# Performance work log

Hardware: AMD Instinct MI355X
Metric: run time of the kernel (lower is better)

## Reference

```python
import jax, jax.numpy as jnp
import numpy as np

N = 50000
BN_EPS = 1e-5


def gcn_conv(x, W, b, src, dst, n):
    # PyG GCNConv: linear transform, add self-loops, symmetric normalization,
    # aggregate messages from src (edge_index[0]) at dst (edge_index[1]).
    x = x @ W
    loop = jnp.arange(n, dtype=src.dtype)
    s = jnp.concatenate([src, loop])
    d = jnp.concatenate([dst, loop])
    ones = jnp.ones(s.shape[0], dtype=x.dtype)
    deg = jax.ops.segment_sum(ones, d, num_segments=n)
    dinv = jnp.where(deg > 0, jax.lax.rsqrt(deg), 0.0)
    norm = dinv[s] * dinv[d]                      # [E+N]
    msg = x[s] * norm[:, None]                    # gather + scale
    out = jax.ops.segment_sum(msg, d, num_segments=n)  # scatter-add
    return out + b


def batch_norm(x, gamma, beta):
    mean = jnp.mean(x, axis=0)
    var = jnp.mean(jnp.square(x - mean), axis=0)  # biased, as torch BN
    return (x - mean) * jax.lax.rsqrt(var + BN_EPS) * gamma + beta


def setup_inputs() -> dict:
    key = jax.random.key(0)
    ks = jax.random.split(key, 4)
    DIN, DH, DOUT, E = 128, 128, 40, 800000
    node_feat = jax.random.normal(ks[0], (N, DIN), dtype=jnp.float32)
    edge_index = jax.random.randint(ks[1], (2, E), 0, N, dtype=jnp.int32)
    W1 = jax.random.normal(ks[2], (DIN, DH), dtype=jnp.float32) / np.sqrt(DIN)
    W2 = jax.random.normal(ks[3], (DH, DOUT), dtype=jnp.float32) / np.sqrt(DH)
    return {
        "node_feat": node_feat,
        "W1": W1,
        "b1": jnp.zeros((DH,), jnp.float32),
        "gamma1": jnp.ones((DH,), jnp.float32),
        "beta1": jnp.zeros((DH,), jnp.float32),
        "W2": W2,
        "b2": jnp.zeros((DOUT,), jnp.float32),
        "edge_index": edge_index,
    }


def reference(node_feat, W1, b1, gamma1, beta1, W2, b2, edge_index):
    src, dst = edge_index[0], edge_index[1]
    x = gcn_conv(node_feat, W1, b1, src, dst, N)
    x = batch_norm(x, gamma1, beta1)
    x = jax.nn.relu(x)
    # dropout is identity at inference
    x = gcn_conv(x, W2, b2, src, dst, N)
    return x
```

## Files before the change

### kernel.cpp

```cpp
#include <hip/hip_runtime.h>

#define NN 50000
#define DIN 128
#define DH  128
#define DOUT 40
#define BN_EPS 1e-5f

__device__ __forceinline__ void atomAddF(float* p, float v) {
  unsafeAtomicAdd(p, v);
}

__global__ void k_deg(const int* __restrict__ dst, int* __restrict__ deg, int E) {
  int e = blockIdx.x * blockDim.x + threadIdx.x;
  if (e < E) atomicAdd(&deg[dst[e]], 1);
}

__global__ void k_off(const int* __restrict__ deg, int* __restrict__ off,
                      int* __restrict__ cur, float* __restrict__ dinv,
                      int* __restrict__ counter) {
  int i = blockIdx.x * 256 + threadIdx.x;
  int lane = threadIdx.x & 63;
  int d = (i < NN) ? deg[i] : 0;
  int pre = d;
#pragma unroll
  for (int o = 1; o < 64; o <<= 1) {
    int v = __shfl_up(pre, o);
    if (lane >= o) pre += v;
  }
  int tot = __shfl(pre, 63);
  int base = 0;
  if (lane == 63) base = atomicAdd(counter, tot);
  base = __shfl(base, 63);
  int o0 = base + pre - d;
  if (i < NN) {
    off[i] = o0; cur[i] = o0;
    dinv[i] = rsqrtf((float)d + 1.0f);
  }
}

__global__ void k_fill(const int* __restrict__ src, const int* __restrict__ dst,
                       int* __restrict__ cur, int* __restrict__ csr, int E) {
  int e = blockIdx.x * blockDim.x + threadIdx.x;
  if (e >= E) return;
  int pos = atomicAdd(&cur[dst[e]], 1);
  csr[pos] = src[e];
}

__global__ __launch_bounds__(256) void k_gemm1(const float* __restrict__ X,
                                               const float* __restrict__ W,
                                               const float* __restrict__ dinv,
                                               float* __restrict__ Y) {
  int t = threadIdx.x;
  int tx = t & 31;
  int ty = t >> 5;
  int r0 = blockIdx.x * 64 + ty * 8;
  int c0 = tx * 4;
  const float4* W4 = (const float4*)W;

  const float* xp[8];
#pragma unroll
  for (int r = 0; r < 8; ++r) {
    int row = r0 + r;
    if (row >= NN) row = NN - 1;
    xp[r] = X + (size_t)row * DIN;
  }

  float acc[8][4] = {};
  for (int k = 0; k < DIN; k += 4) {
    float4 w0 = W4[(k + 0) * 32 + tx];
    float4 w1 = W4[(k + 1) * 32 + tx];
    float4 w2 = W4[(k + 2) * 32 + tx];
    float4 w3 = W4[(k + 3) * 32 + tx];
#pragma unroll
    for (int r = 0; r < 8; ++r) {
      float4 xv = *(const float4*)(xp[r] + k);
      acc[r][0] = fmaf(xv.x, w0.x, fmaf(xv.y, w1.x, fmaf(xv.z, w2.x, fmaf(xv.w, w3.x, acc[r][0]))));
      acc[r][1] = fmaf(xv.x, w0.y, fmaf(xv.y, w1.y, fmaf(xv.z, w2.y, fmaf(xv.w, w3.y, acc[r][1]))));
      acc[r][2] = fmaf(xv.x, w0.z, fmaf(xv.y, w1.z, fmaf(xv.z, w2.z, fmaf(xv.w, w3.z, acc[r][2]))));
      acc[r][3] = fmaf(xv.x, w0.w, fmaf(xv.y, w1.w, fmaf(xv.z, w2.w, fmaf(xv.w, w3.w, acc[r][3]))));
    }
  }
#pragma unroll
  for (int r = 0; r < 8; ++r) {
    int row = r0 + r;
    if (row < NN) {
      float dv = dinv[row];
      *(float4*)(Y + (size_t)row * DH + c0) =
          make_float4(acc[r][0] * dv, acc[r][1] * dv, acc[r][2] * dv, acc[r][3] * dv);
    }
  }
}

__global__ __launch_bounds__(256) void k_pull1(
    const int* __restrict__ off, const int* __restrict__ deg,
    const int* __restrict__ csr, const float* __restrict__ Y1,
    const float* __restrict__ dinv, const float* __restrict__ b1,
    float* __restrict__ Z, float* __restrict__ colsum,
    float* __restrict__ colsumsq) {
  __shared__ float s_sum[4][128], s_sq[4][128];
  int t = threadIdx.x, lane = t & 63, wid = t >> 6;
  const float2* Y = (const float2*)Y1;
  float bx = b1[2 * lane], by = b1[2 * lane + 1];
  float sx = 0.f, sy = 0.f, qx = 0.f, qy = 0.f;
  int n0 = blockIdx.x * 16 + wid * 4;
  for (int u = 0; u < 4; ++u) {
    int n = n0 + u;
    float2 acc = Y[(size_t)n * 64 + lane];
    int o = off[n], dg = deg[n];
    for (int base = 0; base < dg; base += 64) {
      int cnt = min(64, dg - base);
      int myidx = (base + lane < dg) ? csr[o + base + lane] : 0;
      for (int k = 0; k < cnt; ++k) {
        int sN = __shfl(myidx, k);
        float2 y = Y[(size_t)sN * 64 + lane];
        acc.x += y.x; acc.y += y.y;
      }
    }
    float dn = dinv[n];
    float zx = fmaf(dn, acc.x, bx);
    float zy = fmaf(dn, acc.y, by);
    ((float2*)Z)[(size_t)n * 64 + lane] = make_float2(zx, zy);
    sx += zx; sy += zy; qx += zx * zx; qy += zy * zy;
  }
  s_sum[wid][2 * lane] = sx; s_sum[wid][2 * lane + 1] = sy;
  s_sq[wid][2 * lane]  = qx; s_sq[wid][2 * lane + 1]  = qy;
  __syncthreads();
  if (t < 128) {
    atomAddF(&colsum[t],   s_sum[0][t] + s_sum[1][t] + s_sum[2][t] + s_sum[3][t]);
    atomAddF(&colsumsq[t], s_sq[0][t] + s_sq[1][t] + s_sq[2][t] + s_sq[3][t]);
  }
}

__global__ void k_bn(const float* __restrict__ colsum, const float* __restrict__ colsumsq,
                     const float* __restrict__ gamma, const float* __restrict__ beta,
                     float* __restrict__ scale, float* __restrict__ shift) {
  int j = threadIdx.x;
  float mean = colsum[j] * (1.0f / NN);
  float var  = colsumsq[j] * (1.0f / NN) - mean * mean;
  float sc = gamma[j] * rsqrtf(var + BN_EPS);
  scale[j] = sc;
  shift[j] = beta[j] - mean * sc;
}

__global__ __launch_bounds__(256) void k_gemm2(const float* __restrict__ Z,
                                               const float* __restrict__ W2,
                                               const float* __restrict__ scale,
                                               const float* __restrict__ shift,
                                               const float* __restrict__ dinv,
                                               float* __restrict__ Y2) {
  int t = threadIdx.x;
  if (t >= 250) return;
  int tx = t % 10;
  int ty = t / 10;
  int r0 = blockIdx.x * 100 + ty * 4;
  int c0 = tx * 4;
  const float4* W4  = (const float4*)W2;
  const float4* sc4 = (const float4*)scale;
  const float4* sh4 = (const float4*)shift;

  const float* zp[4];
#pragma unroll
  for (int r = 0; r < 4; ++r) zp[r] = Z + (size_t)(r0 + r) * DH;

  float acc[4][4] = {};
  for (int k4 = 0; k4 < DH / 4; ++k4) {
    int k = k4 * 4;
    float4 sc = sc4[k4], sh = sh4[k4];
    float4 w0 = W4[(k + 0) * 10 + tx];
    float4 w1 = W4[(k + 1) * 10 + tx];
    float4 w2 = W4[(k + 2) * 10 + tx];
    float4 w3 = W4[(k + 3) * 10 + tx];
#pragma unroll
    for (int r = 0; r < 4; ++r) {
      float4 zv = *(const float4*)(zp[r] + k);
      float x0 = fmaxf(fmaf(zv.x, sc.x, sh.x), 0.f);
      float x1 = fmaxf(fmaf(zv.y, sc.y, sh.y), 0.f);
      float x2 = fmaxf(fmaf(zv.z, sc.z, sh.z), 0.f);
      float x3 = fmaxf(fmaf(zv.w, sc.w, sh.w), 0.f);
      acc[r][0] = fmaf(x0, w0.x, fmaf(x1, w1.x, fmaf(x2, w2.x, fmaf(x3, w3.x, acc[r][0]))));
      acc[r][1] = fmaf(x0, w0.y, fmaf(x1, w1.y, fmaf(x2, w2.y, fmaf(x3, w3.y, acc[r][1]))));
      acc[r][2] = fmaf(x0, w0.z, fmaf(x1, w1.z, fmaf(x2, w2.z, fmaf(x3, w3.z, acc[r][2]))));
      acc[r][3] = fmaf(x0, w0.w, fmaf(x1, w1.w, fmaf(x2, w2.w, fmaf(x3, w3.w, acc[r][3]))));
    }
  }
#pragma unroll
  for (int r = 0; r < 4; ++r) {
    int row = r0 + r;
    float dv = dinv[row];
    *(float4*)(Y2 + (size_t)row * DOUT + c0) =
        make_float4(acc[r][0] * dv, acc[r][1] * dv, acc[r][2] * dv, acc[r][3] * dv);
  }
}

__global__ __launch_bounds__(256) void k_pull2(
    const int* __restrict__ off, const int* __restrict__ deg,
    const int* __restrict__ csr, const float* __restrict__ Y2,
    const float* __restrict__ dinv, const float* __restrict__ b2,
    float* __restrict__ out) {
  int t = threadIdx.x, lane = t & 63, wid = t >> 6;
  bool act = lane < DOUT;
  float bv = act ? b2[lane] : 0.f;
  int n0 = blockIdx.x * 16 + wid * 4;
  for (int u = 0; u < 4; ++u) {
    int n = n0 + u;
    float acc = act ? Y2[(size_t)n * DOUT + lane] : 0.f;
    int o = off[n], dg = deg[n];
    for (int base = 0; base < dg; base += 64) {
      int cnt = min(64, dg - base);
      int myidx = (base + lane < dg) ? csr[o + base + lane] : 0;
      for (int k = 0; k < cnt; ++k) {
        int sN = __shfl(myidx, k);
        if (act) acc += Y2[(size_t)sN * DOUT + lane];
      }
    }
    if (act) out[(size_t)n * DOUT + lane] = fmaf(dinv[n], acc, bv);
  }
}

extern "C" void kernel_launch(void* const* d_in, const int* in_sizes, int n_in,
                              void* d_out, int out_size, void* d_ws, size_t ws_size,
                              hipStream_t stream) {
  const float* X     = (const float*)d_in[0];
  const float* W1    = (const float*)d_in[1];
  const float* b1    = (const float*)d_in[2];
  const float* gamma = (const float*)d_in[3];
  const float* beta  = (const float*)d_in[4];
  const float* W2    = (const float*)d_in[5];
  const float* b2    = (const float*)d_in[6];
  const int*   edges = (const int*)d_in[7];
  int E = in_sizes[7] / 2;
  const int* src = edges;
  const int* dst = edges + E;

  int E4 = (E + 3) & ~3;
  int* i_deg = (int*)d_ws;
  int* i_off = i_deg + 50048;
  int* i_cur = i_off + 50048;
  int* i_cnt = i_cur + 50016;
  int* i_csr = i_cur + 50048;
  float* f_dinv = (float*)(i_csr + E4);
  float* f_Y1   = f_dinv + 50048;
  float* f_Z    = f_Y1 + (size_t)NN * DH;
  float* f_st   = f_Z + (size_t)NN * DH;
  float* f_Y2   = f_Y1;

  hipMemsetAsync(i_deg, 0, 50000 * sizeof(int), stream);
  hipMemsetAsync(i_cnt, 0, sizeof(int), stream);
  hipMemsetAsync(f_st, 0, 256 * sizeof(float), stream);

  k_deg <<<(E + 255) / 256, 256, 0, stream>>>(dst, i_deg, E);
  k_off <<<(NN + 255) / 256, 256, 0, stream>>>(i_deg, i_off, i_cur, f_dinv, i_cnt);
  k_fill<<<(E + 255) / 256, 256, 0, stream>>>(src, dst, i_cur, i_csr, E);
  k_gemm1<<<(NN + 63) / 64, 256, 0, stream>>>(X, W1, f_dinv, f_Y1);
  k_pull1<<<NN / 16, 256, 0, stream>>>(i_off, i_deg, i_csr, f_Y1, f_dinv, b1,
                                       f_Z, f_st, f_st + 128);
  k_bn<<<1, 128, 0, stream>>>(f_st, f_st + 128, gamma, beta, f_st + 256, f_st + 384);
  k_gemm2<<<500, 256, 0, stream>>>(f_Z, W2, f_st + 256, f_st + 384, f_dinv, f_Y2);
  k_pull2<<<NN / 16, 256, 0, stream>>>(i_off, i_deg, i_csr, f_Y2, f_dinv, b2,
                                       (float*)d_out);
}
```

Before: 432.5 us.

## Store GEMM outputs as bf16 and unroll edge gathers with scalar CSR loads

Both GEMMs now write their dinv-scaled feature rows as bf16 instead of fp32. This halves the bytes the pull kernels gather for every edge. The pull loops drop the shuffle-broadcast of neighbor indices in favor of wave-uniform CSR reads via readfirstlane, unrolled by 8 so several gathers are in flight at once. The cost is bf16 rounding of intermediate messages, which could loosen accuracy against the fp32 reference.

```diff
diff --git a/kernel.cpp b/kernel.cpp
--- a/kernel.cpp
+++ b/kernel.cpp
@@ -8,6 +8,20 @@
 
 __device__ __forceinline__ void atomAddF(float* p, float v) {
   unsafeAtomicAdd(p, v);
+}
+
+__device__ __forceinline__ unsigned short f2bf(float f) {
+  unsigned int u = __float_as_uint(f);
+  return (unsigned short)((u + 0x7FFFu + ((u >> 16) & 1u)) >> 16);
+}
+__device__ __forceinline__ float bflo(unsigned int u) {
+  return __uint_as_float(u << 16);
+}
+__device__ __forceinline__ float bfhi(unsigned int u) {
+  return __uint_as_float(u & 0xFFFF0000u);
+}
+__device__ __forceinline__ float bf1(unsigned short h) {
+  return __uint_as_float(((unsigned int)h) << 16);
 }
 
 __global__ void k_deg(const int* __restrict__ dst, int* __restrict__ deg, int E) {
@@ -49,7 +63,7 @@
 __global__ __launch_bounds__(256) void k_gemm1(const float* __restrict__ X,
                                                const float* __restrict__ W,
                                                const float* __restrict__ dinv,
-                                               float* __restrict__ Y) {
+                                               unsigned short* __restrict__ Y) {
   int t = threadIdx.x;
   int tx = t & 31;
   int ty = t >> 5;
@@ -85,36 +99,58 @@
     int row = r0 + r;
     if (row < NN) {
       float dv = dinv[row];
-      *(float4*)(Y + (size_t)row * DH + c0) =
-          make_float4(acc[r][0] * dv, acc[r][1] * dv, acc[r][2] * dv, acc[r][3] * dv);
+      ushort4 st;
+      st.x = f2bf(acc[r][0] * dv); st.y = f2bf(acc[r][1] * dv);
+      st.z = f2bf(acc[r][2] * dv); st.w = f2bf(acc[r][3] * dv);
+      *(ushort4*)(Y + (size_t)row * DH + c0) = st;
     }
   }
 }
 
 __global__ __launch_bounds__(256) void k_pull1(
     const int* __restrict__ off, const int* __restrict__ deg,
-    const int* __restrict__ csr, const float* __restrict__ Y1,
+    const int* __restrict__ csr, const unsigned int* __restrict__ Yu,
     const float* __restrict__ dinv, const float* __restrict__ b1,
     float* __restrict__ Z, float* __restrict__ colsum,
     float* __restrict__ colsumsq) {
   __shared__ float s_sum[4][128], s_sq[4][128];
   int t = threadIdx.x, lane = t & 63, wid = t >> 6;
-  const float2* Y = (const float2*)Y1;
   float bx = b1[2 * lane], by = b1[2 * lane + 1];
   float sx = 0.f, sy = 0.f, qx = 0.f, qy = 0.f;
   int n0 = blockIdx.x * 16 + wid * 4;
   for (int u = 0; u < 4; ++u) {
     int n = n0 + u;
-    float2 acc = Y[(size_t)n * 64 + lane];
-    int o = off[n], dg = deg[n];
-    for (int base = 0; base < dg; base += 64) {
-      int cnt = min(64, dg - base);
-      int myidx = (base + lane < dg) ? csr[o + base + lane] : 0;
-      for (int k = 0; k < cnt; ++k) {
-        int sN = __shfl(myidx, k);
-        float2 y = Y[(size_t)sN * 64 + lane];
-        acc.x += y.x; acc.y += y.y;
-      }
+    unsigned int us = Yu[(size_t)n * 64 + lane];
+    float2 acc = make_float2(bflo(us), bfhi(us));
+    int o  = __builtin_amdgcn_readfirstlane(off[n]);
+    int dg = __builtin_amdgcn_readfirstlane(deg[n]);
+    int kb = 0;
+    for (; kb + 8 <= dg; kb += 8) {
+      int s0 = csr[o + kb + 0], s1 = csr[o + kb + 1];
+      int s2 = csr[o + kb + 2], s3 = csr[o + kb + 3];
+      int s4 = csr[o + kb + 4], s5 = csr[o + kb + 5];
+      int s6 = csr[o + kb + 6], s7 = csr[o + kb + 7];
+      unsigned int y0 = Yu[(size_t)s0 * 64 + lane];
+      unsigned int y1 = Yu[(size_t)s1 * 64 + lane];
+      unsigned int y2 = Yu[(size_t)s2 * 64 + lane];
+      unsigned int y3 = Yu[(size_t)s3 * 64 + lane];
+      unsigned int y4 = Yu[(size_t)s4 * 64 + lane];
+      unsigned int y5 = Yu[(size_t)s5 * 64 + lane];
+      unsigned int y6 = Yu[(size_t)s6 * 64 + lane];
+      unsigned int y7 = Yu[(size_t)s7 * 64 + lane];
+      acc.x += bflo(y0); acc.y += bfhi(y0);
+      acc.x += bflo(y1); acc.y += bfhi(y1);
+      acc.x += bflo(y2); acc.y += bfhi(y2);
+      acc.x += bflo(y3); acc.y += bfhi(y3);
+      acc.x += bflo(y4); acc.y += bfhi(y4);
+      acc.x += bflo(y5); acc.y += bfhi(y5);
+      acc.x += bflo(y6); acc.y += bfhi(y6);
+      acc.x += bflo(y7); acc.y += bfhi(y7);
+    }
+    for (int k = kb; k < dg; ++k) {
+      int sN = csr[o + k];
+      unsigned int y = Yu[(size_t)sN * 64 + lane];
+      acc.x += bflo(y); acc.y += bfhi(y);
     }
     float dn = dinv[n];
     float zx = fmaf(dn, acc.x, bx);
@@ -147,7 +183,7 @@
                                                const float* __restrict__ scale,
                                                const float* __restrict__ shift,
                                                const float* __restrict__ dinv,
-                                               float* __restrict__ Y2) {
+                                               unsigned short* __restrict__ Y2) {
   int t = threadIdx.x;
   if (t >= 250) return;
   int tx = t % 10;
@@ -187,31 +223,48 @@
   for (int r = 0; r < 4; ++r) {
     int row = r0 + r;
     float dv = dinv[row];
-    *(float4*)(Y2 + (size_t)row * DOUT + c0) =
-        make_float4(acc[r][0] * dv, acc[r][1] * dv, acc[r][2] * dv, acc[r][3] * dv);
+    ushort4 st;
+    st.x = f2bf(acc[r][0] * dv); st.y = f2bf(acc[r][1] * dv);
+    st.z = f2bf(acc[r][2] * dv); st.w = f2bf(acc[r][3] * dv);
+    *(ushort4*)(Y2 + (size_t)row * DOUT + c0) = st;
   }
 }
 
 __global__ __launch_bounds__(256) void k_pull2(
     const int* __restrict__ off, const int* __restrict__ deg,
-    const int* __restrict__ csr, const float* __restrict__ Y2,
+    const int* __restrict__ csr, const unsigned short* __restrict__ Y2,
     const float* __restrict__ dinv, const float* __restrict__ b2,
     float* __restrict__ out) {
   int t = threadIdx.x, lane = t & 63, wid = t >> 6;
   bool act = lane < DOUT;
   float bv = act ? b2[lane] : 0.f;
+  int lx = act ? lane : 0;
   int n0 = blockIdx.x * 16 + wid * 4;
   for (int u = 0; u < 4; ++u) {
     int n = n0 + u;
-    float acc = act ? Y2[(size_t)n * DOUT + lane] : 0.f;
-    int o = off[n], dg = deg[n];
-    for (int base = 0; base < dg; base += 64) {
-      int cnt = min(64, dg - base);
-      int myidx = (base + lane < dg) ? csr[o + base + lane] : 0;
-      for (int k = 0; k < cnt; ++k) {
-        int sN = __shfl(myidx, k);
-        if (act) acc += Y2[(size_t)sN * DOUT + lane];
-      }
+    float acc = bf1(Y2[(size_t)n * DOUT + lx]);
+    int o  = __builtin_amdgcn_readfirstlane(off[n]);
+    int dg = __builtin_amdgcn_readfirstlane(deg[n]);
+    int kb = 0;
+    for (; kb + 8 <= dg; kb += 8) {
+      int s0 = csr[o + kb + 0], s1 = csr[o + kb + 1];
+      int s2 = csr[o + kb + 2], s3 = csr[o + kb + 3];
+      int s4 = csr[o + kb + 4], s5 = csr[o + kb + 5];
+      int s6 = csr[o + kb + 6], s7 = csr[o + kb + 7];
+      unsigned short y0 = Y2[(size_t)s0 * DOUT + lx];
+      unsigned short y1 = Y2[(size_t)s1 * DOUT + lx];
+      unsigned short y2 = Y2[(size_t)s2 * DOUT + lx];
+      unsigned short y3 = Y2[(size_t)s3 * DOUT + lx];
+      unsigned short y4 = Y2[(size_t)s4 * DOUT + lx];
+      unsigned short y5 = Y2[(size_t)s5 * DOUT + lx];
+      unsigned short y6 = Y2[(size_t)s6 * DOUT + lx];
+      unsigned short y7 = Y2[(size_t)s7 * DOUT + lx];
+      acc += bf1(y0); acc += bf1(y1); acc += bf1(y2); acc += bf1(y3);
+      acc += bf1(y4); acc += bf1(y5); acc += bf1(y6); acc += bf1(y7);
+    }
+    for (int k = kb; k < dg; ++k) {
+      int sN = csr[o + k];
+      acc += bf1(Y2[(size_t)sN * DOUT + lx]);
     }
     if (act) out[(size_t)n * DOUT + lane] = fmaf(dinv[n], acc, bv);
   }
@@ -239,10 +292,10 @@
   int* i_cnt = i_cur + 50016;
   int* i_csr = i_cur + 50048;
   float* f_dinv = (float*)(i_csr + E4);
-  float* f_Y1   = f_dinv + 50048;
-  float* f_Z    = f_Y1 + (size_t)NN * DH;
-  float* f_st   = f_Z + (size_t)NN * DH;
-  float* f_Y2   = f_Y1;
+  unsigned short* u_Y1 = (unsigned short*)(f_dinv + 50048);
+  float* f_Z  = (float*)(u_Y1 + (size_t)NN * DH);
+  float* f_st = f_Z + (size_t)NN * DH;
+  unsigned short* u_Y2 = u_Y1;
 
   hipMemsetAsync(i_deg, 0, 50000 * sizeof(int), stream);
   hipMemsetAsync(i_cnt, 0, sizeof(int), stream);
@@ -251,11 +304,12 @@
   k_deg <<<(E + 255) / 256, 256, 0, stream>>>(dst, i_deg, E);
   k_off <<<(NN + 255) / 256, 256, 0, stream>>>(i_deg, i_off, i_cur, f_dinv, i_cnt);
   k_fill<<<(E + 255) / 256, 256, 0, stream>>>(src, dst, i_cur, i_csr, E);
-  k_gemm1<<<(NN + 63) / 64, 256, 0, stream>>>(X, W1, f_dinv, f_Y1);
-  k_pull1<<<NN / 16, 256, 0, stream>>>(i_off, i_deg, i_csr, f_Y1, f_dinv, b1,
+  k_gemm1<<<(NN + 63) / 64, 256, 0, stream>>>(X, W1, f_dinv, u_Y1);
+  k_pull1<<<NN / 16, 256, 0, stream>>>(i_off, i_deg, i_csr,
+                                       (const unsigned int*)u_Y1, f_dinv, b1,
                                        f_Z, f_st, f_st + 128);
   k_bn<<<1, 128, 0, stream>>>(f_st, f_st + 128, gamma, beta, f_st + 256, f_st + 384);
-  k_gemm2<<<500, 256, 0, stream>>>(f_Z, W2, f_st + 256, f_st + 384, f_dinv, f_Y2);
-  k_pull2<<<NN / 16, 256, 0, stream>>>(i_off, i_deg, i_csr, f_Y2, f_dinv, b2,
+  k_gemm2<<<500, 256, 0, stream>>>(f_Z, W2, f_st + 256, f_st + 384, f_dinv, u_Y2);
+  k_pull2<<<NN / 16, 256, 0, stream>>>(i_off, i_deg, i_csr, u_Y2, f_dinv, b2,
                                        (float*)d_out);
 }
```

Result: faster. 380.1 us (-12.1%).

## Store transformed features in bf16 and gather multiple nodes per wavefront

Applied to the files above, without the earlier changes.

The GEMM outputs Y1 and Y2 are now stored as bf16, which halves the bytes gathered per edge in both aggregation kernels. The pull kernels are restructured so each wavefront handles four nodes (layer 1) or two nodes (layer 2) at once, with 16-byte or 4-byte vector loads per lane. Loops are padded to the max degree within the wave, and the CSR buffer gets slack for the padded index reads. The cost is reduced precision in the intermediate features and some divergence from the degree imbalance between nodes sharing a wave.

```diff
diff --git a/kernel.cpp b/kernel.cpp
--- a/kernel.cpp
+++ b/kernel.cpp
@@ -8,6 +8,17 @@
 
 __device__ __forceinline__ void atomAddF(float* p, float v) {
   unsafeAtomicAdd(p, v);
+}
+
+__device__ __forceinline__ unsigned short f2bf(float f) {
+  unsigned int u = __float_as_uint(f);
+  return (unsigned short)((u + 0x7FFFu + ((u >> 16) & 1u)) >> 16);
+}
+__device__ __forceinline__ float bflo(unsigned int u) {
+  return __uint_as_float(u << 16);
+}
+__device__ __forceinline__ float bfhi(unsigned int u) {
+  return __uint_as_float(u & 0xFFFF0000u);
 }
 
 __global__ void k_deg(const int* __restrict__ dst, int* __restrict__ deg, int E) {
@@ -49,7 +60,7 @@
 __global__ __launch_bounds__(256) void k_gemm1(const float* __restrict__ X,
                                                const float* __restrict__ W,
                                                const float* __restrict__ dinv,
-                                               float* __restrict__ Y) {
+                                               unsigned short* __restrict__ Y) {
   int t = threadIdx.x;
   int tx = t & 31;
   int ty = t >> 5;
@@ -85,45 +96,77 @@
     int row = r0 + r;
     if (row < NN) {
       float dv = dinv[row];
-      *(float4*)(Y + (size_t)row * DH + c0) =
-          make_float4(acc[r][0] * dv, acc[r][1] * dv, acc[r][2] * dv, acc[r][3] * dv);
+      ushort4 st;
+      st.x = f2bf(acc[r][0] * dv); st.y = f2bf(acc[r][1] * dv);
+      st.z = f2bf(acc[r][2] * dv); st.w = f2bf(acc[r][3] * dv);
+      *(ushort4*)(Y + (size_t)row * DH + c0) = st;
     }
   }
 }
 
 __global__ __launch_bounds__(256) void k_pull1(
     const int* __restrict__ off, const int* __restrict__ deg,
-    const int* __restrict__ csr, const float* __restrict__ Y1,
+    const int* __restrict__ csr, const uint4* __restrict__ Yq,
     const float* __restrict__ dinv, const float* __restrict__ b1,
     float* __restrict__ Z, float* __restrict__ colsum,
     float* __restrict__ colsumsq) {
   __shared__ float s_sum[4][128], s_sq[4][128];
-  int t = threadIdx.x, lane = t & 63, wid = t >> 6;
-  const float2* Y = (const float2*)Y1;
-  float bx = b1[2 * lane], by = b1[2 * lane + 1];
-  float sx = 0.f, sy = 0.f, qx = 0.f, qy = 0.f;
-  int n0 = blockIdx.x * 16 + wid * 4;
-  for (int u = 0; u < 4; ++u) {
-    int n = n0 + u;
-    float2 acc = Y[(size_t)n * 64 + lane];
-    int o = off[n], dg = deg[n];
-    for (int base = 0; base < dg; base += 64) {
-      int cnt = min(64, dg - base);
-      int myidx = (base + lane < dg) ? csr[o + base + lane] : 0;
-      for (int k = 0; k < cnt; ++k) {
-        int sN = __shfl(myidx, k);
-        float2 y = Y[(size_t)sN * 64 + lane];
-        acc.x += y.x; acc.y += y.y;
+  int t = threadIdx.x, l = t & 63, wid = t >> 6;
+  int sub = l & 15;
+  int n = blockIdx.x * 16 + wid * 4 + (l >> 4);
+
+  uint4 ys = Yq[(size_t)n * 16 + sub];
+  float a0 = bflo(ys.x), a1 = bfhi(ys.x), a2 = bflo(ys.y), a3 = bfhi(ys.y);
+  float a4 = bflo(ys.z), a5 = bfhi(ys.z), a6 = bflo(ys.w), a7 = bfhi(ys.w);
+
+  int o = off[n], dg = deg[n];
+  int mr = max(dg, __shfl_xor(dg, 16));
+  mr = max(mr, __shfl_xor(mr, 32));
+
+  for (int kb = 0; kb < mr; kb += 16) {
+    int pos = kb + sub;
+    int myidx = csr[o + ((pos < dg) ? pos : 0)];
+    int rem = dg - kb;
+    int kmax = mr - kb; if (kmax > 16) kmax = 16;
+    for (int kk = 0; kk < kmax; ++kk) {
+      int sN = __shfl(myidx, (l & 48) + kk);
+      if (kk < rem) {
+        uint4 y = Yq[(size_t)sN * 16 + sub];
+        a0 += bflo(y.x); a1 += bfhi(y.x);
+        a2 += bflo(y.y); a3 += bfhi(y.y);
+        a4 += bflo(y.z); a5 += bfhi(y.z);
+        a6 += bflo(y.w); a7 += bfhi(y.w);
       }
     }
-    float dn = dinv[n];
-    float zx = fmaf(dn, acc.x, bx);
-    float zy = fmaf(dn, acc.y, by);
-    ((float2*)Z)[(size_t)n * 64 + lane] = make_float2(zx, zy);
-    sx += zx; sy += zy; qx += zx * zx; qy += zy * zy;
-  }
-  s_sum[wid][2 * lane] = sx; s_sum[wid][2 * lane + 1] = sy;
-  s_sq[wid][2 * lane]  = qx; s_sq[wid][2 * lane + 1]  = qy;
+  }
+
+  float dn = dinv[n];
+  const float4* b4 = (const float4*)b1;
+  float4 bA = b4[sub * 2], bB = b4[sub * 2 + 1];
+  float z0 = fmaf(dn, a0, bA.x), z1 = fmaf(dn, a1, bA.y);
+  float z2 = fmaf(dn, a2, bA.z), z3 = fmaf(dn, a3, bA.w);
+  float z4 = fmaf(dn, a4, bB.x), z5 = fmaf(dn, a5, bB.y);
+  float z6 = fmaf(dn, a6, bB.z), z7 = fmaf(dn, a7, bB.w);
+  float4* Z4 = (float4*)Z;
+  Z4[(size_t)n * 32 + sub * 2 + 0] = make_float4(z0, z1, z2, z3);
+  Z4[(size_t)n * 32 + sub * 2 + 1] = make_float4(z4, z5, z6, z7);
+
+  float s[8] = {z0, z1, z2, z3, z4, z5, z6, z7};
+  float q[8];
+#pragma unroll
+  for (int j = 0; j < 8; ++j) q[j] = s[j] * s[j];
+#pragma unroll
+  for (int j = 0; j < 8; ++j) {
+    s[j] += __shfl_xor(s[j], 16); s[j] += __shfl_xor(s[j], 32);
+    q[j] += __shfl_xor(q[j], 16); q[j] += __shfl_xor(q[j], 32);
+  }
+  if (l < 16) {
+#pragma unroll
+    for (int j = 0; j < 8; ++j) {
+      s_sum[wid][sub * 8 + j] = s[j];
+      s_sq[wid][sub * 8 + j]  = q[j];
+    }
+  }
   __syncthreads();
   if (t < 128) {
     atomAddF(&colsum[t],   s_sum[0][t] + s_sum[1][t] + s_sum[2][t] + s_sum[3][t]);
@@ -147,7 +190,7 @@
                                                const float* __restrict__ scale,
                                                const float* __restrict__ shift,
                                                const float* __restrict__ dinv,
-                                               float* __restrict__ Y2) {
+                                               unsigned short* __restrict__ Y2) {
   int t = threadIdx.x;
   if (t >= 250) return;
   int tx = t % 10;
@@ -187,33 +230,49 @@
   for (int r = 0; r < 4; ++r) {
     int row = r0 + r;
     float dv = dinv[row];
-    *(float4*)(Y2 + (size_t)row * DOUT + c0) =
-        make_float4(acc[r][0] * dv, acc[r][1] * dv, acc[r][2] * dv, acc[r][3] * dv);
+    ushort4 st;
+    st.x = f2bf(acc[r][0] * dv); st.y = f2bf(acc[r][1] * dv);
+    st.z = f2bf(acc[r][2] * dv); st.w = f2bf(acc[r][3] * dv);
+    *(ushort4*)(Y2 + (size_t)row * DOUT + c0) = st;
   }
 }
 
 __global__ __launch_bounds__(256) void k_pull2(
     const int* __restrict__ off, const int* __restrict__ deg,
-    const int* __restrict__ csr, const float* __restrict__ Y2,
+    const int* __restrict__ csr, const unsigned int* __restrict__ Yu2,
     const float* __restrict__ dinv, const float* __restrict__ b2,
     float* __restrict__ out) {
-  int t = threadIdx.x, lane = t & 63, wid = t >> 6;
-  bool act = lane < DOUT;
-  float bv = act ? b2[lane] : 0.f;
-  int n0 = blockIdx.x * 16 + wid * 4;
-  for (int u = 0; u < 4; ++u) {
-    int n = n0 + u;
-    float acc = act ? Y2[(size_t)n * DOUT + lane] : 0.f;
-    int o = off[n], dg = deg[n];
-    for (int base = 0; base < dg; base += 64) {
-      int cnt = min(64, dg - base);
-      int myidx = (base + lane < dg) ? csr[o + base + lane] : 0;
-      for (int k = 0; k < cnt; ++k) {
-        int sN = __shfl(myidx, k);
-        if (act) acc += Y2[(size_t)sN * DOUT + lane];
+  int t = threadIdx.x, l = t & 63, wid = t >> 6;
+  int il = l & 31;
+  int n = blockIdx.x * 8 + wid * 2 + (l >> 5);
+  bool act = il < 20;
+  int c0 = il * 2;
+
+  float a0 = 0.f, a1 = 0.f;
+  if (act) {
+    unsigned int us = Yu2[(size_t)n * 20 + il];
+    a0 = bflo(us); a1 = bfhi(us);
+  }
+  int o = off[n], dg = deg[n];
+  int mr = max(dg, __shfl_xor(dg, 32));
+
+  for (int kb = 0; kb < mr; kb += 32) {
+    int pos = kb + il;
+    int myidx = csr[o + ((pos < dg) ? pos : 0)];
+    int rem = dg - kb;
+    int kmax = mr - kb; if (kmax > 32) kmax = 32;
+    for (int kk = 0; kk < kmax; ++kk) {
+      int sN = __shfl(myidx, (l & 32) + kk);
+      if (act && kk < rem) {
+        unsigned int y = Yu2[(size_t)sN * 20 + il];
+        a0 += bflo(y); a1 += bfhi(y);
       }
     }
-    if (act) out[(size_t)n * DOUT + lane] = fmaf(dinv[n], acc, bv);
+  }
+  if (act) {
+    float dn = dinv[n];
+    float2 r = make_float2(fmaf(dn, a0, b2[c0]), fmaf(dn, a1, b2[c0 + 1]));
+    ((float2*)(out + (size_t)n * DOUT))[il] = r;
   }
 }
 
@@ -232,17 +291,17 @@
   const int* src = edges;
   const int* dst = edges + E;
 
-  int E4 = (E + 3) & ~3;
+  int E4 = ((E + 64) + 3) & ~3;
   int* i_deg = (int*)d_ws;
   int* i_off = i_deg + 50048;
   int* i_cur = i_off + 50048;
   int* i_cnt = i_cur + 50016;
   int* i_csr = i_cur + 50048;
   float* f_dinv = (float*)(i_csr + E4);
-  float* f_Y1   = f_dinv + 50048;
-  float* f_Z    = f_Y1 + (size_t)NN * DH;
-  float* f_st   = f_Z + (size_t)NN * DH;
-  float* f_Y2   = f_Y1;
+  unsigned short* u_Y1 = (unsigned short*)(f_dinv + 50048);
+  float* f_Z  = (float*)(u_Y1 + (size_t)NN * DH);
+  float* f_st = f_Z + (size_t)NN * DH;
+  unsigned short* u_Y2 = u_Y1;
 
   hipMemsetAsync(i_deg, 0, 50000 * sizeof(int), stream);
   hipMemsetAsync(i_cnt, 0, sizeof(int), stream);
@@ -251,11 +310,13 @@
   k_deg <<<(E + 255) / 256, 256, 0, stream>>>(dst, i_deg, E);
   k_off <<<(NN + 255) / 256, 256, 0, stream>>>(i_deg, i_off, i_cur, f_dinv, i_cnt);
   k_fill<<<(E + 255) / 256, 256, 0, stream>>>(src, dst, i_cur, i_csr, E);
-  k_gemm1<<<(NN + 63) / 64, 256, 0, stream>>>(X, W1, f_dinv, f_Y1);
-  k_pull1<<<NN / 16, 256, 0, stream>>>(i_off, i_deg, i_csr, f_Y1, f_dinv, b1,
+  k_gemm1<<<(NN + 63) / 64, 256, 0, stream>>>(X, W1, f_dinv, u_Y1);
+  k_pull1<<<NN / 16, 256, 0, stream>>>(i_off, i_deg, i_csr,
+                                       (const uint4*)u_Y1, f_dinv, b1,
                                        f_Z, f_st, f_st + 128);
   k_bn<<<1, 128, 0, stream>>>(f_st, f_st + 128, gamma, beta, f_st + 256, f_st + 384);
-  k_gemm2<<<500, 256, 0, stream>>>(f_Z, W2, f_st + 256, f_st + 384, f_dinv, f_Y2);
-  k_pull2<<<NN / 16, 256, 0, stream>>>(i_off, i_deg, i_csr, f_Y2, f_dinv, b2,
-                                       (float*)d_out);
-}
+  k_gemm2<<<500, 256, 0, stream>>>(f_Z, W2, f_st + 256, f_st + 384, f_dinv, u_Y2);
+  k_pull2<<<NN / 8, 256, 0, stream>>>(i_off, i_deg, i_csr,
+                                      (const unsigned int*)u_Y2, f_dinv, b2,
+                                      (float*)d_out);
+}
```

Measured after the change: 390.4 us. 1.11x faster.
